# Performance work log

Measured on AMD Instinct MI355X. Metric: run time of the kernel, lower is better.

The kernel has to match this reference:

```python
import jax, jax.numpy as jnp
import numpy as np

N_NODES = 100000
MAX_DEG = 64
NODE_DIM = 256
V = 8192
NUM_SAMPLES = 16


def setup_inputs() -> dict:
    key = jax.random.key(0)
    k1, k2, k3, k4 = jax.random.split(key, 4)
    ids = jax.random.randint(k1, (V,), 0, N_NODES, dtype=jnp.int32)
    adj_info = jax.random.randint(k2, (N_NODES, MAX_DEG), 0, N_NODES, dtype=jnp.int32)
    features = jax.random.normal(k3, (N_NODES, NODE_DIM), dtype=jnp.float32)
    W = jax.random.normal(k4, (NODE_DIM, NODE_DIM), dtype=jnp.float32) * 0.05
    b = jnp.zeros((NODE_DIM,), dtype=jnp.float32)
    return {"ids": ids, "adj_info": adj_info, "features": features, "W": W, "b": b,
            "num_samples": NUM_SAMPLES}


def reference(ids, adj_info, features, W, b, num_samples):
    n_nodes, neig_num = adj_info.shape
    group_dim = neig_num // num_samples
    K = group_dim * num_samples  # tf.slice to a multiple of num_samples
    v = ids.shape[0]

    adj_lists = adj_info[ids][:, :K]                     # [V, K] neighbor ids
    v_f = features[ids]                                  # [V, d]
    n_f = features[adj_lists]                            # [V, K, d]

    # linear sampler branch: dense(v_f) then matmul with neighbor feats, relu
    l = v_f @ W + b                                      # [V, d]
    scores = jax.nn.relu(jnp.einsum('vd,vkd->vk', l, n_f))  # [V, K]

    # grouped argmin: pick one neighbor per group of group_dim
    scores = scores.reshape(v, num_samples, group_dim)   # [V, S, G]
    idx_y = jnp.argmin(scores, axis=-1).astype(jnp.int32)  # [V, S]
    idx_y = idx_y + (jnp.arange(num_samples, dtype=jnp.int32) * group_dim)[None, :]

    sel = jnp.take_along_axis(adj_lists, idx_y, axis=1)  # [V, S]

    # count non-padding neighbors (padding sentinel = n_nodes - 1)
    nonpad = jnp.where(sel == n_nodes - 1,
                       jnp.zeros(sel.shape, jnp.float32),
                       jnp.ones(sel.shape, jnp.float32))
    numnz = nonpad.sum(axis=1)                           # [V]
    att = jnp.ones(sel.shape, jnp.float32)
    return sel, att, numnz, numnz
```

## Files before the change

kernel.cpp:

```cpp
#include <hip/hip_runtime.h>
#include <hip/hip_bf16.h>

#define N_NODES   100000
#define MAX_DEG   64
#define NODE_DIM  256
#define NUM_V     8192
#define NSAMP     16
#define GROUP_DIM 4
#define SENTINEL  (N_NODES - 1)

__global__ __launch_bounds__(256) void fused_sampler_kernel(
    const int* __restrict__ ids,
    const int* __restrict__ adj,
    const float* __restrict__ features,
    const float* __restrict__ W,
    const float* __restrict__ bias,
    float* __restrict__ out_sel,
    float* __restrict__ out_att,
    float* __restrict__ out_nz1,
    float* __restrict__ out_nz2) {
  __shared__ float f_s[NODE_DIM];
  __shared__ float l_s[NODE_DIM];
  __shared__ int   adj_s[MAX_DEG];
  __shared__ float nz_s[NSAMP];

  const int v   = blockIdx.x;
  const int tid = threadIdx.x;
  const int nid = ids[v];

  f_s[tid] = features[(size_t)nid * NODE_DIM + tid];
  if (tid < MAX_DEG) adj_s[tid] = adj[(size_t)nid * MAX_DEG + tid];
  __syncthreads();

  {
    float acc = 0.0f;
#pragma unroll 8
    for (int k = 0; k < NODE_DIM; ++k) {
      acc += f_s[k] * W[(size_t)k * NODE_DIM + tid];
    }
    l_s[tid] = acc + bias[tid];
  }
  __syncthreads();

  const int wave = tid >> 6;
  const int lane = tid & 63;
  const int q    = lane >> 2;
  const int sub  = lane & 3;
  const int k    = wave * 16 + q;

  const int nb = adj_s[k];
  const float* __restrict__ rowp = features + (size_t)nb * NODE_DIM + sub * 4;
  const float* __restrict__ lp   = l_s + sub * 4;

  float p = 0.0f;
#pragma unroll
  for (int c = 0; c < 16; ++c) {
    const float4 f  = *reinterpret_cast<const float4*>(rowp + c * 16);
    const float4 lv = *reinterpret_cast<const float4*>(lp + c * 16);
    p += f.x * lv.x + f.y * lv.y + f.z * lv.z + f.w * lv.w;
  }
  p += __shfl_xor(p, 1, 64);
  p += __shfl_xor(p, 2, 64);
  float s = p > 0.0f ? p : 0.0f;

  int g = q & 3;
  {
    float os = __shfl_xor(s, 4, 64);
    int   og = __shfl_xor(g, 4, 64);
    if (os < s || (os == s && og < g)) { s = os; g = og; }
    os = __shfl_xor(s, 8, 64);
    og = __shfl_xor(g, 8, 64);
    if (os < s || (os == s && og < g)) { s = os; g = og; }
  }

  if ((lane & 15) == 0) {
    const int gl    = lane >> 4;
    const int s_idx = wave * 4 + gl;
    const int selid = adj_s[s_idx * GROUP_DIM + g];
    out_sel[(size_t)v * NSAMP + s_idx] = (float)selid;
    out_att[(size_t)v * NSAMP + s_idx] = 1.0f;
    nz_s[s_idx] = (selid == SENTINEL) ? 0.0f : 1.0f;
  }
  __syncthreads();

  if (tid == 0) {
    float nz = 0.0f;
#pragma unroll
    for (int t = 0; t < NSAMP; ++t) nz += nz_s[t];
    out_nz1[v] = nz;
    out_nz2[v] = nz;
  }
}

extern "C" void kernel_launch(void* const* d_in, const int* in_sizes, int n_in,
                              void* d_out, int out_size, void* d_ws,
                              size_t ws_size, hipStream_t stream) {
  const int*   ids      = (const int*)d_in[0];
  const int*   adj      = (const int*)d_in[1];
  const float* features = (const float*)d_in[2];
  const float* W        = (const float*)d_in[3];
  const float* bias     = (const float*)d_in[4];

  float* out     = (float*)d_out;
  float* out_sel = out;
  float* out_att = out + (size_t)NUM_V * NSAMP;
  float* out_nz1 = out + (size_t)2 * NUM_V * NSAMP;
  float* out_nz2 = out_nz1 + NUM_V;

  fused_sampler_kernel<<<NUM_V, 256, 0, stream>>>(
      ids, adj, features, W, bias, out_sel, out_att, out_nz1, out_nz2);
}
```

Measured before the change: 282.2 us.

## Process eight vertices per block to reuse W loads across the dense layer

Each block now handles eight vertices instead of one. W rows are loaded once per block and applied to all eight feature vectors held in shared memory, which cuts global W traffic by about eight times. The neighbor-scoring loop then runs over the eight vertices one after another. The grid is eight times smaller (1024 blocks), so less latency is hidden per block on the gather phase, and each thread uses more registers.

```diff
diff --git a/kernel.cpp b/kernel.cpp
--- a/kernel.cpp
+++ b/kernel.cpp
@@ -9,6 +9,8 @@
 #define GROUP_DIM 4
 #define SENTINEL  (N_NODES - 1)
 
+#define VPB 8
+
 __global__ __launch_bounds__(256) void fused_sampler_kernel(
     const int* __restrict__ ids,
     const int* __restrict__ adj,
@@ -19,26 +21,59 @@
     float* __restrict__ out_att,
     float* __restrict__ out_nz1,
     float* __restrict__ out_nz2) {
-  __shared__ float f_s[NODE_DIM];
-  __shared__ float l_s[NODE_DIM];
-  __shared__ int   adj_s[MAX_DEG];
-  __shared__ float nz_s[NSAMP];
+  __shared__ float f_s[VPB][NODE_DIM];
+  __shared__ float l_s[VPB][NODE_DIM];
+  __shared__ int   adj_s[VPB][MAX_DEG];
+  __shared__ float nz_s[VPB][NSAMP];
+  __shared__ int   nid_s[VPB];
 
-  const int v   = blockIdx.x;
   const int tid = threadIdx.x;
-  const int nid = ids[v];
+  const int v0  = blockIdx.x * VPB;
 
-  f_s[tid] = features[(size_t)nid * NODE_DIM + tid];
-  if (tid < MAX_DEG) adj_s[tid] = adj[(size_t)nid * MAX_DEG + tid];
+  if (tid < VPB) nid_s[tid] = ids[v0 + tid];
   __syncthreads();
 
   {
-    float acc = 0.0f;
-#pragma unroll 8
-    for (int k = 0; k < NODE_DIM; ++k) {
-      acc += f_s[k] * W[(size_t)k * NODE_DIM + tid];
+    const int i0 = tid;
+    const int i1 = tid + 256;
+    const int vi0 = i0 >> 6, d0 = (i0 & 63) * 4;
+    const int vi1 = i1 >> 6, d1 = (i1 & 63) * 4;
+    *reinterpret_cast<float4*>(&f_s[vi0][d0]) =
+        *reinterpret_cast<const float4*>(
+            &features[(size_t)nid_s[vi0] * NODE_DIM + d0]);
+    *reinterpret_cast<float4*>(&f_s[vi1][d1]) =
+        *reinterpret_cast<const float4*>(
+            &features[(size_t)nid_s[vi1] * NODE_DIM + d1]);
+  }
+  {
+    const int i0 = tid, i1 = tid + 256;
+    adj_s[i0 >> 6][i0 & 63] =
+        adj[(size_t)nid_s[i0 >> 6] * MAX_DEG + (i0 & 63)];
+    adj_s[i1 >> 6][i1 & 63] =
+        adj[(size_t)nid_s[i1 >> 6] * MAX_DEG + (i1 & 63)];
+  }
+  __syncthreads();
+
+  {
+    float acc[VPB] = {};
+#pragma unroll 2
+    for (int k4 = 0; k4 < NODE_DIM; k4 += 4) {
+      const float w0 = W[(size_t)(k4 + 0) * NODE_DIM + tid];
+      const float w1 = W[(size_t)(k4 + 1) * NODE_DIM + tid];
+      const float w2 = W[(size_t)(k4 + 2) * NODE_DIM + tid];
+      const float w3 = W[(size_t)(k4 + 3) * NODE_DIM + tid];
+#pragma unroll
+      for (int vi = 0; vi < VPB; ++vi) {
+        const float4 f = *reinterpret_cast<const float4*>(&f_s[vi][k4]);
+        acc[vi] += f.x * w0;
+        acc[vi] += f.y * w1;
+        acc[vi] += f.z * w2;
+        acc[vi] += f.w * w3;
+      }
     }
-    l_s[tid] = acc + bias[tid];
+    const float bv = bias[tid];
+#pragma unroll
+    for (int vi = 0; vi < VPB; ++vi) l_s[vi][tid] = acc[vi] + bv;
   }
   __syncthreads();
 
@@ -46,49 +81,54 @@
   const int lane = tid & 63;
   const int q    = lane >> 2;
   const int sub  = lane & 3;
-  const int k    = wave * 16 + q;
+  const int kslot = wave * 16 + q;
 
-  const int nb = adj_s[k];
-  const float* __restrict__ rowp = features + (size_t)nb * NODE_DIM + sub * 4;
-  const float* __restrict__ lp   = l_s + sub * 4;
+#pragma unroll 1
+  for (int vi = 0; vi < VPB; ++vi) {
+    const int nb = adj_s[vi][kslot];
+    const float* __restrict__ rowp =
+        features + (size_t)nb * NODE_DIM + sub * 4;
+    const float* __restrict__ lp = &l_s[vi][sub * 4];
 
-  float p = 0.0f;
+    float p = 0.0f;
 #pragma unroll
-  for (int c = 0; c < 16; ++c) {
-    const float4 f  = *reinterpret_cast<const float4*>(rowp + c * 16);
-    const float4 lv = *reinterpret_cast<const float4*>(lp + c * 16);
-    p += f.x * lv.x + f.y * lv.y + f.z * lv.z + f.w * lv.w;
-  }
-  p += __shfl_xor(p, 1, 64);
-  p += __shfl_xor(p, 2, 64);
-  float s = p > 0.0f ? p : 0.0f;
+    for (int c = 0; c < 16; ++c) {
+      const float4 f  = *reinterpret_cast<const float4*>(rowp + c * 16);
+      const float4 lv = *reinterpret_cast<const float4*>(lp + c * 16);
+      p += f.x * lv.x + f.y * lv.y + f.z * lv.z + f.w * lv.w;
+    }
+    p += __shfl_xor(p, 1, 64);
+    p += __shfl_xor(p, 2, 64);
+    float s = p > 0.0f ? p : 0.0f;
 
-  int g = q & 3;
-  {
-    float os = __shfl_xor(s, 4, 64);
-    int   og = __shfl_xor(g, 4, 64);
-    if (os < s || (os == s && og < g)) { s = os; g = og; }
-    os = __shfl_xor(s, 8, 64);
-    og = __shfl_xor(g, 8, 64);
-    if (os < s || (os == s && og < g)) { s = os; g = og; }
-  }
+    int g = q & 3;
+    {
+      float os = __shfl_xor(s, 4, 64);
+      int   og = __shfl_xor(g, 4, 64);
+      if (os < s || (os == s && og < g)) { s = os; g = og; }
+      os = __shfl_xor(s, 8, 64);
+      og = __shfl_xor(g, 8, 64);
+      if (os < s || (os == s && og < g)) { s = os; g = og; }
+    }
 
-  if ((lane & 15) == 0) {
-    const int gl    = lane >> 4;
-    const int s_idx = wave * 4 + gl;
-    const int selid = adj_s[s_idx * GROUP_DIM + g];
-    out_sel[(size_t)v * NSAMP + s_idx] = (float)selid;
-    out_att[(size_t)v * NSAMP + s_idx] = 1.0f;
-    nz_s[s_idx] = (selid == SENTINEL) ? 0.0f : 1.0f;
+    if ((lane & 15) == 0) {
+      const int gl    = lane >> 4;
+      const int s_idx = wave * 4 + gl;
+      const int selid = adj_s[vi][s_idx * GROUP_DIM + g];
+      const int vv    = v0 + vi;
+      out_sel[(size_t)vv * NSAMP + s_idx] = (float)selid;
+      out_att[(size_t)vv * NSAMP + s_idx] = 1.0f;
+      nz_s[vi][s_idx] = (selid == SENTINEL) ? 0.0f : 1.0f;
+    }
   }
   __syncthreads();
 
-  if (tid == 0) {
+  if (tid < VPB) {
     float nz = 0.0f;
 #pragma unroll
-    for (int t = 0; t < NSAMP; ++t) nz += nz_s[t];
-    out_nz1[v] = nz;
-    out_nz2[v] = nz;
+    for (int t = 0; t < NSAMP; ++t) nz += nz_s[tid][t];
+    out_nz1[v0 + tid] = nz;
+    out_nz2[v0 + tid] = nz;
   }
 }
 
@@ -107,6 +147,6 @@
   float* out_nz1 = out + (size_t)2 * NUM_V * NSAMP;
   float* out_nz2 = out_nz1 + NUM_V;
 
-  fused_sampler_kernel<<<NUM_V, 256, 0, stream>>>(
+  fused_sampler_kernel<<<NUM_V / VPB, 256, 0, stream>>>(
       ids, adj, features, W, bias, out_sel, out_att, out_nz1, out_nz2);
 }
```

Measured after the change: 235.4 us. 16.6% less time.
